# Kernel optimization log

Hardware: AMD Instinct MI355X
Metric: run time of the kernel (lower is better)

## Reference

```python
import jax, jax.numpy as jnp
import numpy as np

N = 100000      # nodes
E = 1600000     # edges (avg degree 16)
F_IN = 128
H = 64
OUT = 1
NEG_SLOPE = 0.2  # PyG GATConv default negative_slope


def setup_inputs() -> dict:
    key = jax.random.key(0)
    ks = jax.random.split(key, 20)
    inp = {
        "x": jax.random.normal(ks[0], (N, F_IN), dtype=jnp.float32),
        "edge_index": jax.random.randint(ks[1], (2, E), 0, N, dtype=jnp.int64),
        "edge_weight": jax.random.uniform(ks[2], (E,), dtype=jnp.float32),
    }
    # GATConv params: W [in,out], att_src [out], att_dst [out], bias [out]
    dims = [(F_IN, H), (H, H), (H, H), (H, OUT)]
    names = ["0", "1", "2", "l"]
    ki = 3
    for nm, (fi, fo) in zip(names, dims):
        s = 1.0 / np.sqrt(fi)
        inp["W" + nm] = jax.random.normal(ks[ki], (fi, fo), dtype=jnp.float32) * s; ki += 1
        inp["as" + nm] = jax.random.normal(ks[ki], (fo,), dtype=jnp.float32) * 0.1; ki += 1
        inp["ad" + nm] = jax.random.normal(ks[ki], (fo,), dtype=jnp.float32) * 0.1; ki += 1
        inp["b" + nm] = jnp.zeros((fo,), dtype=jnp.float32)
    return inp


def gat_conv(x, src, dst, W, a_s, a_d, b, n):
    # h = W x  (single head)
    h = x @ W                                   # [N, F_out]
    e_src = h @ a_s                             # [N] per-node src attention term
    e_dst = h @ a_d                             # [N] per-node dst attention term
    e = jax.nn.leaky_relu(e_src[src] + e_dst[dst], NEG_SLOPE)   # [E+N]
    # segment softmax over incoming edges of each dst node (self-loops ensure non-empty)
    m = jax.ops.segment_max(e, dst, num_segments=n)
    ex = jnp.exp(e - m[dst])
    denom = jax.ops.segment_sum(ex, dst, num_segments=n)
    alpha = ex / (denom[dst] + 1e-16)
    # scatter-add aggregation of alpha-weighted source features
    out = jax.ops.segment_sum(h[src] * alpha[:, None], dst, num_segments=n)
    return out + b


def reference(x, edge_index, edge_weight,
              W0, as0, ad0, b0,
              W1, as1, ad1, b1,
              W2, as2, ad2, b2,
              Wl, asl, adl, bl):
    # eval mode: F.dropout(training=False) is identity; edge_weight unused by GATConv
    n = x.shape[0]
    loop = jnp.arange(n, dtype=edge_index.dtype)
    src = jnp.concatenate([edge_index[0], loop])   # add_self_loops=True
    dst = jnp.concatenate([edge_index[1], loop])
    for (W, a_s, a_d, b) in [(W0, as0, ad0, b0), (W1, as1, ad1, b1), (W2, as2, ad2, b2)]:
        x = jax.nn.relu(gat_conv(x, src, dst, W, a_s, a_d, b, n))
    return gat_conv(x, src, dst, Wl, asl, adl, bl, n)
```

## Files before the change

### kernel.cpp

```cpp
#include <hip/hip_runtime.h>
#include <hip/hip_bf16.h>
#include <math.h>

#define CAP 64


__global__ __launch_bounds__(256) void fill_part_kernel(
        const int* __restrict__ ei, int* __restrict__ deg,
        int* __restrict__ col, int E, int nchunk) {
    int part = blockIdx.x & 7;
    int chunk = blockIdx.x >> 3;
    int per = (E + nchunk - 1) / nchunk;
    int lo = chunk * per;
    int hi = lo + per; if (hi > E) hi = E;
    for (int idx = lo + threadIdx.x; idx < hi; idx += 256) {
        int d = ei[E + idx];
        if (((d >> 4) & 7) == part) {
            int s = ei[idx];
            int pos = atomicAdd(&deg[d], 1);
            if (pos < CAP - 1) col[(size_t)d * CAP + pos] = s;
        }
    }
}


__device__ __forceinline__ float rl(float v, int l) {
    return __int_as_float(__builtin_amdgcn_readlane(__float_as_int(v), l));
}

template<int K>
__global__ __launch_bounds__(256, 2) void gemm_h_kernel(
        const float* __restrict__ x, const float* __restrict__ W,
        const float* __restrict__ a_s, const float* __restrict__ a_d,
        float* __restrict__ h, float* __restrict__ es, float* __restrict__ ed, int n) {
    constexpr int K4 = K / 4;
    constexpr int RW = 8;
    constexpr int NLD = RW * K4 / 64;

    int tid = threadIdx.x;
    int lane = tid & 63;
    float w[K];
    #pragma unroll
    for (int k = 0; k < K; ++k) w[k] = W[k * 64 + lane];
    float asv = a_s[lane];
    float adv = a_d[lane];

    int wid = (blockIdx.x * 256 + tid) >> 6;
    int nwaves = (gridDim.x * 256) >> 6;
    int ngroups = (n + RW - 1) / RW;

    for (int g = wid; g < ngroups; g += nwaves) {
        int r0 = g * RW;
        float4 xr[NLD];
        #pragma unroll
        for (int i = 0; i < NLD; ++i) {
            int flat = i * 64 + lane;
            int r = flat / K4, k4 = flat % K4;
            int row = r0 + r; if (row >= n) row = n - 1;
            xr[i] = *(const float4*)(x + (size_t)row * K + k4 * 4);
        }
        #pragma unroll
        for (int r = 0; r < RW; ++r) {
            float acc0 = 0.f, acc1 = 0.f, acc2 = 0.f, acc3 = 0.f;
            #pragma unroll
            for (int k4 = 0; k4 < K4; ++k4) {
                int flat = r * K4 + k4;
                int reg = flat >> 6, src = flat & 63;
                float4 v = xr[reg];
                acc0 = fmaf(rl(v.x, src), w[4 * k4 + 0], acc0);
                acc1 = fmaf(rl(v.y, src), w[4 * k4 + 1], acc1);
                acc2 = fmaf(rl(v.z, src), w[4 * k4 + 2], acc2);
                acc3 = fmaf(rl(v.w, src), w[4 * k4 + 3], acc3);
            }
            int row = r0 + r;
            float a = (acc0 + acc1) + (acc2 + acc3);
            float ps = a * asv;
            float pd = a * adv;
            #pragma unroll
            for (int off = 32; off; off >>= 1) {
                ps += __shfl_xor(ps, off);
                pd += __shfl_xor(pd, off);
            }
            if (row < n) {
                h[(size_t)row * 64 + lane] = a;
                if (lane == 0) { es[row] = ps; ed[row] = pd; }
            }
        }
    }
}


template<bool PROJ>
__global__ __launch_bounds__(256) void aggregate64_kernel(
        const float* __restrict__ h, const float* __restrict__ es, const float* __restrict__ ed,
        const int* __restrict__ deg, const int* __restrict__ col,
        const float* __restrict__ bias, float* __restrict__ xout, int n, int do_relu,
        const float* __restrict__ Wl, float* __restrict__ hl) {
    int lane = threadIdx.x & 63;
    int node = (blockIdx.x * blockDim.x + threadIdx.x) >> 6;
    if (node >= n) return;
    int cr = deg[node]; if (cr > CAP - 1) cr = CAP - 1;
    int cnt = cr + 1;
    float edi = ed[node];

    int s = 0;
    float e = -INFINITY;
    if (lane < cr) {
        s = col[(size_t)node * CAP + lane];
        float t = es[s] + edi;
        e = (t >= 0.f) ? t : 0.2f * t;
    } else if (lane == cr) {
        s = node;
        float t = es[node] + edi;
        e = (t >= 0.f) ? t : 0.2f * t;
    }
    float m = e;
    #pragma unroll
    for (int off = 32; off; off >>= 1) m = fmaxf(m, __shfl_xor(m, off));
    float p = __expf(e - m);
    float denom = p;
    #pragma unroll
    for (int off = 32; off; off >>= 1) denom += __shfl_xor(denom, off);

    float a0 = 0.f, a1 = 0.f, a2 = 0.f, a3 = 0.f;
    float a4 = 0.f, a5 = 0.f, a6 = 0.f, a7 = 0.f;
    int iters = (cnt + 7) & ~7;
    for (int j = 0; j < iters; j += 8) {
        float p0 = __shfl(p, j + 0); int s0 = __shfl(s, j + 0);
        float p1 = __shfl(p, j + 1); int s1 = __shfl(s, j + 1);
        float p2 = __shfl(p, j + 2); int s2 = __shfl(s, j + 2);
        float p3 = __shfl(p, j + 3); int s3 = __shfl(s, j + 3);
        float p4 = __shfl(p, j + 4); int s4 = __shfl(s, j + 4);
        float p5 = __shfl(p, j + 5); int s5 = __shfl(s, j + 5);
        float p6 = __shfl(p, j + 6); int s6 = __shfl(s, j + 6);
        float p7 = __shfl(p, j + 7); int s7 = __shfl(s, j + 7);
        a0 = fmaf(p0, h[(s0 << 6) | lane], a0);
        a1 = fmaf(p1, h[(s1 << 6) | lane], a1);
        a2 = fmaf(p2, h[(s2 << 6) | lane], a2);
        a3 = fmaf(p3, h[(s3 << 6) | lane], a3);
        a4 = fmaf(p4, h[(s4 << 6) | lane], a4);
        a5 = fmaf(p5, h[(s5 << 6) | lane], a5);
        a6 = fmaf(p6, h[(s6 << 6) | lane], a6);
        a7 = fmaf(p7, h[(s7 << 6) | lane], a7);
    }
    float o = (((a0 + a1) + (a2 + a3)) + ((a4 + a5) + (a6 + a7))) / denom + bias[lane];
    if (do_relu) o = fmaxf(o, 0.f);
    if constexpr (PROJ) {
        float ph = o * Wl[lane];
        #pragma unroll
        for (int off = 32; off; off >>= 1) ph += __shfl_xor(ph, off);
        if (lane == 0) hl[node] = ph;
    } else {
        xout[(size_t)node * 64 + lane] = o;
    }
}


__global__ __launch_bounds__(256) void aggregate1_kernel(
        const float* __restrict__ hl, const float* __restrict__ asl,
        const float* __restrict__ adl, const float* __restrict__ bl,
        const int* __restrict__ deg, const int* __restrict__ col,
        float* __restrict__ out, int n) {
    int lane = threadIdx.x & 63;
    int node = (blockIdx.x * blockDim.x + threadIdx.x) >> 6;
    if (node >= n) return;
    float As = asl[0], Ad = adl[0], B = bl[0];
    int cr = deg[node]; if (cr > CAP - 1) cr = CAP - 1;
    float edi = hl[node] * Ad;

    float hs = 0.f;
    float e = -INFINITY;
    if (lane < cr) {
        int s = col[(size_t)node * CAP + lane];
        hs = hl[s];
        float t = fmaf(hs, As, edi);
        e = (t >= 0.f) ? t : 0.2f * t;
    } else if (lane == cr) {
        hs = hl[node];
        float t = fmaf(hs, As, edi);
        e = (t >= 0.f) ? t : 0.2f * t;
    }
    float m = e;
    #pragma unroll
    for (int off = 32; off; off >>= 1) m = fmaxf(m, __shfl_xor(m, off));
    float p = __expf(e - m);
    float d = p;
    float a = p * hs;
    #pragma unroll
    for (int off = 32; off; off >>= 1) {
        d += __shfl_xor(d, off);
        a += __shfl_xor(a, off);
    }
    if (lane == 0) out[node] = a / d + B;
}


extern "C" void kernel_launch(void* const* d_in, const int* in_sizes, int n_in,
                              void* d_out, int out_size, void* d_ws, size_t ws_size,
                              hipStream_t stream) {
    const float* x0  = (const float*)d_in[0];
    const int*   ei  = (const int*)d_in[1];
    const float* W0  = (const float*)d_in[3];
    const float* as0 = (const float*)d_in[4];
    const float* ad0 = (const float*)d_in[5];
    const float* b0  = (const float*)d_in[6];
    const float* W1  = (const float*)d_in[7];
    const float* as1 = (const float*)d_in[8];
    const float* ad1 = (const float*)d_in[9];
    const float* b1  = (const float*)d_in[10];
    const float* W2  = (const float*)d_in[11];
    const float* as2 = (const float*)d_in[12];
    const float* ad2 = (const float*)d_in[13];
    const float* b2  = (const float*)d_in[14];
    const float* Wl  = (const float*)d_in[15];
    const float* asl = (const float*)d_in[16];
    const float* adl = (const float*)d_in[17];
    const float* bl  = (const float*)d_in[18];

    int n = in_sizes[0] / 128;
    int E = in_sizes[1] / 2;

    char* p = (char*)d_ws;
    auto alloc = [&](size_t bytes) { char* r = p; p += (bytes + 255) & ~255ULL; return r; };
    float* h   = (float*)alloc((size_t)n * 64 * 4);
    float* xb  = (float*)alloc((size_t)n * 64 * 4);
    int*   col = (int*)alloc((size_t)n * CAP * 4);
    float* es  = (float*)alloc((size_t)n * 4);
    float* ed  = (float*)alloc((size_t)n * 4);
    float* hl  = (float*)alloc((size_t)n * 4);
    int*   deg = (int*)alloc((size_t)n * 4);
    (void)ws_size; (void)n_in; (void)out_size;

    int agg_blocks = (n + 3) / 4;

    hipMemsetAsync(deg, 0, (size_t)n * 4, stream);
    fill_part_kernel<<<8 * 512, 256, 0, stream>>>(ei, deg, col, E, 512);

    gemm_h_kernel<128><<<2048, 256, 0, stream>>>(x0, W0, as0, ad0, h, es, ed, n);
    aggregate64_kernel<false><<<agg_blocks, 256, 0, stream>>>(h, es, ed, deg, col, b0,
                                                              xb, n, 1, nullptr, nullptr);
    gemm_h_kernel<64><<<2048, 256, 0, stream>>>(xb, W1, as1, ad1, h, es, ed, n);
    aggregate64_kernel<false><<<agg_blocks, 256, 0, stream>>>(h, es, ed, deg, col, b1,
                                                              xb, n, 1, nullptr, nullptr);
    gemm_h_kernel<64><<<2048, 256, 0, stream>>>(xb, W2, as2, ad2, h, es, ed, n);
    aggregate64_kernel<true><<<agg_blocks, 256, 0, stream>>>(h, es, ed, deg, col, b2,
                                                             nullptr, n, 1, Wl, hl);
    aggregate1_kernel<<<agg_blocks, 256, 0, stream>>>(hl, asl, adl, bl, deg, col,
                                                      (float*)d_out, n);
}
```

Measured before the change: 443.2 us.

## Compute node projection GEMM with split-bf16 MFMA instead of scalar FMA

Replaces the readlane-based scalar FMA GEMM with MFMA 16x16x32 bf16 instructions, using a hi/lo bf16 split of both x and W (three products) to keep accuracy close to fp32. W fragments are converted once per block into shared memory, each wave handles one 16-row tile, and the attention dot products are reduced across 16 lanes. The grid becomes one wave per tile instead of a fixed 2048 blocks. Each block pays for the W conversion and extra conversion ALU work, and the three-product split only approximates full fp32 precision.

New measurement: 370.7 us. -16.3%, faster.

```diff
diff --git a/kernel.cpp b/kernel.cpp
--- a/kernel.cpp
+++ b/kernel.cpp
@@ -3,6 +3,18 @@
 #include <math.h>
 
 #define CAP 64
+
+typedef __attribute__((ext_vector_type(8))) short bf16x8;
+typedef __attribute__((ext_vector_type(4))) float f32x4;
+
+__device__ __forceinline__ short f2b(float f) {
+    unsigned u = __float_as_uint(f);
+    unsigned r = (u + 0x7FFFu + ((u >> 16) & 1u)) >> 16;
+    return (short)r;
+}
+__device__ __forceinline__ float b2f(short b) {
+    return __uint_as_float(((unsigned)(unsigned short)b) << 16);
+}
 
 
 __global__ __launch_bounds__(256) void fill_part_kernel(
@@ -24,67 +36,100 @@
 }
 
 
-__device__ __forceinline__ float rl(float v, int l) {
-    return __int_as_float(__builtin_amdgcn_readlane(__float_as_int(v), l));
-}
-
 template<int K>
-__global__ __launch_bounds__(256, 2) void gemm_h_kernel(
+__global__ __launch_bounds__(256) void gemm_mfma_kernel(
         const float* __restrict__ x, const float* __restrict__ W,
         const float* __restrict__ a_s, const float* __restrict__ a_d,
         float* __restrict__ h, float* __restrict__ es, float* __restrict__ ed, int n) {
-    constexpr int K4 = K / 4;
-    constexpr int RW = 8;
-    constexpr int NLD = RW * K4 / 64;
+    constexpr int NK = K / 32;
+    __shared__ short bfrag[2 * 4 * NK * 64 * 8];
+    constexpr int HALF = 4 * NK * 64 * 8;
 
     int tid = threadIdx.x;
     int lane = tid & 63;
-    float w[K];
-    #pragma unroll
-    for (int k = 0; k < K; ++k) w[k] = W[k * 64 + lane];
-    float asv = a_s[lane];
-    float adv = a_d[lane];
+    int l15 = lane & 15;
+    int lg = lane >> 4;
+
+    if (tid < 64) {
+        for (int nf = 0; nf < 4; ++nf) {
+            for (int ks = 0; ks < NK; ++ks) {
+                int base = ((nf * NK + ks) * 64 + lane) * 8;
+                #pragma unroll
+                for (int j = 0; j < 8; ++j) {
+                    float wv = W[(ks * 32 + lg * 8 + j) * 64 + nf * 16 + l15];
+                    short hb = f2b(wv);
+                    bfrag[base + j] = hb;
+                    bfrag[HALF + base + j] = f2b(wv - b2f(hb));
+                }
+            }
+        }
+    }
+    __syncthreads();
+
+    float asv[4], adv[4];
+    #pragma unroll
+    for (int nf = 0; nf < 4; ++nf) {
+        asv[nf] = a_s[nf * 16 + l15];
+        adv[nf] = a_d[nf * 16 + l15];
+    }
 
     int wid = (blockIdx.x * 256 + tid) >> 6;
-    int nwaves = (gridDim.x * 256) >> 6;
-    int ngroups = (n + RW - 1) / RW;
-
-    for (int g = wid; g < ngroups; g += nwaves) {
-        int r0 = g * RW;
-        float4 xr[NLD];
-        #pragma unroll
-        for (int i = 0; i < NLD; ++i) {
-            int flat = i * 64 + lane;
-            int r = flat / K4, k4 = flat % K4;
-            int row = r0 + r; if (row >= n) row = n - 1;
-            xr[i] = *(const float4*)(x + (size_t)row * K + k4 * 4);
-        }
-        #pragma unroll
-        for (int r = 0; r < RW; ++r) {
-            float acc0 = 0.f, acc1 = 0.f, acc2 = 0.f, acc3 = 0.f;
+    int nw = (gridDim.x * 256) >> 6;
+    int ntiles = (n + 15) / 16;
+
+    for (int t = wid; t < ntiles; t += nw) {
+        int row0 = t * 16;
+        int row = row0 + l15; if (row >= n) row = n - 1;
+        const float* xr = x + (size_t)row * K + lg * 8;
+
+        bf16x8 ahi[NK], alo[NK];
+        #pragma unroll
+        for (int ks = 0; ks < NK; ++ks) {
+            float4 v0 = *(const float4*)(xr + ks * 32);
+            float4 v1 = *(const float4*)(xr + ks * 32 + 4);
+            float xv[8] = {v0.x, v0.y, v0.z, v0.w, v1.x, v1.y, v1.z, v1.w};
             #pragma unroll
-            for (int k4 = 0; k4 < K4; ++k4) {
-                int flat = r * K4 + k4;
-                int reg = flat >> 6, src = flat & 63;
-                float4 v = xr[reg];
-                acc0 = fmaf(rl(v.x, src), w[4 * k4 + 0], acc0);
-                acc1 = fmaf(rl(v.y, src), w[4 * k4 + 1], acc1);
-                acc2 = fmaf(rl(v.z, src), w[4 * k4 + 2], acc2);
-                acc3 = fmaf(rl(v.w, src), w[4 * k4 + 3], acc3);
-            }
-            int row = r0 + r;
-            float a = (acc0 + acc1) + (acc2 + acc3);
-            float ps = a * asv;
-            float pd = a * adv;
+            for (int j = 0; j < 8; ++j) {
+                short hb = f2b(xv[j]);
+                ahi[ks][j] = hb;
+                alo[ks][j] = f2b(xv[j] - b2f(hb));
+            }
+        }
+
+        f32x4 accs[4];
+        #pragma unroll
+        for (int nf = 0; nf < 4; ++nf) {
+            f32x4 acc = {0.f, 0.f, 0.f, 0.f};
             #pragma unroll
-            for (int off = 32; off; off >>= 1) {
+            for (int ks = 0; ks < NK; ++ks) {
+                bf16x8 bh = *(bf16x8*)&bfrag[((nf * NK + ks) * 64 + lane) * 8];
+                bf16x8 bl = *(bf16x8*)&bfrag[HALF + ((nf * NK + ks) * 64 + lane) * 8];
+                acc = __builtin_amdgcn_mfma_f32_16x16x32_bf16(ahi[ks], bh, acc, 0, 0, 0);
+                acc = __builtin_amdgcn_mfma_f32_16x16x32_bf16(ahi[ks], bl, acc, 0, 0, 0);
+                acc = __builtin_amdgcn_mfma_f32_16x16x32_bf16(alo[ks], bh, acc, 0, 0, 0);
+            }
+            accs[nf] = acc;
+        }
+
+        #pragma unroll
+        for (int r = 0; r < 4; ++r) {
+            int orow = row0 + lg * 4 + r;
+            float ps = 0.f, pd = 0.f;
+            if (orow < n) {
+                #pragma unroll
+                for (int nf = 0; nf < 4; ++nf) {
+                    float hv = accs[nf][r];
+                    h[(size_t)orow * 64 + nf * 16 + l15] = hv;
+                    ps = fmaf(hv, asv[nf], ps);
+                    pd = fmaf(hv, adv[nf], pd);
+                }
+            }
+            #pragma unroll
+            for (int off = 8; off; off >>= 1) {
                 ps += __shfl_xor(ps, off);
                 pd += __shfl_xor(pd, off);
             }
-            if (row < n) {
-                h[(size_t)row * 64 + lane] = a;
-                if (lane == 0) { es[row] = ps; ed[row] = pd; }
-            }
+            if (l15 == 0 && orow < n) { es[orow] = ps; ed[orow] = pd; }
         }
     }
 }
@@ -232,17 +277,19 @@
     (void)ws_size; (void)n_in; (void)out_size;
 
     int agg_blocks = (n + 3) / 4;
+    int ntiles = (n + 15) / 16;
+    int gemm_blocks = (ntiles + 3) / 4;
 
     hipMemsetAsync(deg, 0, (size_t)n * 4, stream);
     fill_part_kernel<<<8 * 512, 256, 0, stream>>>(ei, deg, col, E, 512);
 
-    gemm_h_kernel<128><<<2048, 256, 0, stream>>>(x0, W0, as0, ad0, h, es, ed, n);
+    gemm_mfma_kernel<128><<<gemm_blocks, 256, 0, stream>>>(x0, W0, as0, ad0, h, es, ed, n);
     aggregate64_kernel<false><<<agg_blocks, 256, 0, stream>>>(h, es, ed, deg, col, b0,
                                                               xb, n, 1, nullptr, nullptr);
-    gemm_h_kernel<64><<<2048, 256, 0, stream>>>(xb, W1, as1, ad1, h, es, ed, n);
+    gemm_mfma_kernel<64><<<gemm_blocks, 256, 0, stream>>>(xb, W1, as1, ad1, h, es, ed, n);
     aggregate64_kernel<false><<<agg_blocks, 256, 0, stream>>>(h, es, ed, deg, col, b1,
                                                               xb, n, 1, nullptr, nullptr);
-    gemm_h_kernel<64><<<2048, 256, 0, stream>>>(xb, W2, as2, ad2, h, es, ed, n);
+    gemm_mfma_kernel<64><<<gemm_blocks, 256, 0, stream>>>(xb, W2, as2, ad2, h, es, ed, n);
     aggregate64_kernel<true><<<agg_blocks, 256, 0, stream>>>(h, es, ed, deg, col, b2,
                                                              nullptr, n, 1, Wl, hl);
     aggregate1_kernel<<<agg_blocks, 256, 0, stream>>>(hl, asl, adl, bl, deg, col,
```
